# Kernel optimization log

Hardware: AMD Instinct MI355X
Metric: run time of the kernel (lower is better)

The kernel has to match this reference:

```python
import jax, jax.numpy as jnp
import numpy as np

N_NEWS, N_ENT, N_TOP = 100000, 50000, 2000
D = 128
N_EDGES = 1600000
HID, OUT = 512, 128


def setup_inputs() -> dict:
    key = jax.random.key(0)
    ks = jax.random.split(key, 12)
    return {
        "news_feats": jax.random.normal(ks[0], (N_NEWS, D), jnp.float32),
        "entity_feats": jax.random.normal(ks[1], (N_ENT, D), jnp.float32),
        "topic_feats": jax.random.normal(ks[2], (N_TOP, D), jnp.float32),
        "ent_row": jax.random.randint(ks[3], (N_EDGES,), 0, N_NEWS, jnp.int32),
        "ent_col": jax.random.randint(ks[4], (N_EDGES,), 0, N_ENT, jnp.int32),
        "top_row": jax.random.randint(ks[5], (N_EDGES,), 0, N_NEWS, jnp.int32),
        "top_col": jax.random.randint(ks[6], (N_EDGES,), 0, N_TOP, jnp.int32),
        "W1": jax.random.normal(ks[7], (3 * D, HID), jnp.float32) * 0.05,
        "b1": jnp.zeros((HID,), jnp.float32),
        "W2": jax.random.normal(ks[8], (HID, OUT), jnp.float32) * 0.05,
        "b2": jnp.zeros((OUT,), jnp.float32),
    }


def _agg(feats, row, col, num_news):
    # SpMM with binary adjacency: sum neighbor feats per news node
    gathered = feats[col]                                   # [E, D]
    summed = jax.ops.segment_sum(gathered, row, num_segments=num_news)
    deg = jax.ops.segment_sum(jnp.ones_like(row, dtype=feats.dtype), row,
                              num_segments=num_news)
    return summed / (deg[:, None] + 1e-8)


def reference(news_feats, entity_feats, topic_feats, ent_row, ent_col,
              top_row, top_col, W1, b1, W2, b2):
    n = news_feats.shape[0]
    ent_agg = _agg(entity_feats, ent_row, ent_col, n)
    top_agg = _agg(topic_feats, top_row, top_col, n)
    out = jnp.concatenate([news_feats, ent_agg, top_agg], axis=1)  # [N, 3D]
    h = jnp.tanh(out @ W1 + b1)
    return h @ W2 + b2
```

## Files before the change

kernel.cpp:

```cpp
#include <hip/hip_runtime.h>
#include <hip/hip_bf16.h>

#define NN 100000
#define NE 50000
#define NT 2000
#define DD 128
#define NEDGE 1600000
#define HID 512
#define OUTD 128
#define K1 (3*DD)
#define KX 256
#define NBKT 391

typedef __bf16 bf16x8 __attribute__((ext_vector_type(8)));
typedef __bf16 bf16x4 __attribute__((ext_vector_type(4)));
typedef float  f32x4  __attribute__((ext_vector_type(4)));

__device__ __forceinline__ __bf16 f2b(float f) {
    __hip_bfloat16 h = __float2bfloat16(f);
    union { __hip_bfloat16 h; __bf16 b; } u; u.h = h; return u.b;
}

__device__ __forceinline__ void gll16(const void* g, void* l) {
    __builtin_amdgcn_global_load_lds((const __attribute__((address_space(1))) void*)g,
                                     (__attribute__((address_space(3))) void*)l, 16, 0, 0);
}

__device__ __forceinline__ float ftanh(float x) {
    x = fminf(fmaxf(x, -15.f), 15.f);
    float t = __expf(2.f * x);
    return (t - 1.f) / (t + 1.f);
}

__global__ void conv_feats(const float* __restrict__ entf, const float* __restrict__ topf,
                           __bf16* __restrict__ entb, __bf16* __restrict__ topb) {
    long i = ((long)blockIdx.x * 256 + threadIdx.x) * 4;
    const long NEL = (long)NE * DD;
    if (i < NEL) {
        float4 v = *(const float4*)(entf + i);
        *(bf16x4*)(entb + i) = bf16x4{f2b(v.x), f2b(v.y), f2b(v.z), f2b(v.w)};
    } else {
        long j = i - NEL;
        float4 v = *(const float4*)(topf + j);
        *(bf16x4*)(topb + j) = bf16x4{f2b(v.x), f2b(v.y), f2b(v.z), f2b(v.w)};
    }
}

__global__ __launch_bounds__(256) void hist_buckets(const int* __restrict__ er,
                                                    const int* __restrict__ tr,
                                                    int* __restrict__ bc_e,
                                                    int* __restrict__ bc_t) {
    __shared__ int lhe[NBKT], lht[NBKT];
    const int tid = threadIdx.x;
    for (int i = tid; i < NBKT; i += 256) { lhe[i] = 0; lht[i] = 0; }
    __syncthreads();
    const int base = blockIdx.x * 8192;
    #pragma unroll 4
    for (int k = 0; k < 32; k++) {
        int e = base + k * 256 + tid;
        if (e < NEDGE) {
            atomicAdd(&lhe[er[e] >> 8], 1);
            atomicAdd(&lht[tr[e] >> 8], 1);
        }
    }
    __syncthreads();
    for (int i = tid; i < NBKT; i += 256) {
        if (lhe[i]) atomicAdd(&bc_e[i], lhe[i]);
        if (lht[i]) atomicAdd(&bc_t[i], lht[i]);
    }
}

__global__ void scan_buckets(int* __restrict__ bc_e, int* __restrict__ bc_t,
                             int* __restrict__ cur_e, int* __restrict__ cur_t,
                             int* __restrict__ offs_e, int* __restrict__ offs_t) {
    int* bc  = blockIdx.y ? bc_t : bc_e;
    int* cur = blockIdx.y ? cur_t : cur_e;
    int* offs = blockIdx.y ? offs_t : offs_e;
    __shared__ int s[512];
    int i = threadIdx.x;
    s[i] = (i < NBKT) ? bc[i] : 0;
    __syncthreads();
    #pragma unroll
    for (int off = 1; off < 512; off <<= 1) {
        int v = (i >= off) ? s[i - off] : 0;
        __syncthreads();
        s[i] += v;
        __syncthreads();
    }
    if (i < NBKT) {
        bc[i] = s[i];
        cur[i] = i ? s[i - 1] : 0;
    }
    if (i == 0) offs[0] = 0;
}

__global__ __launch_bounds__(256) void scatter_bucket(const int* __restrict__ er,
                                                      const int* __restrict__ ec,
                                                      const int* __restrict__ tr,
                                                      const int* __restrict__ tc,
                                                      int* __restrict__ cur_e,
                                                      int* __restrict__ cur_t,
                                                      int* __restrict__ be,
                                                      int* __restrict__ bt) {
    __shared__ int lhe[NBKT], lht[NBKT];
    __shared__ int lbe[NBKT], lbt[NBKT];
    const int tid = threadIdx.x;
    for (int i = tid; i < NBKT; i += 256) { lhe[i] = 0; lht[i] = 0; }
    __syncthreads();
    const int base = blockIdx.x * 4096;
    #pragma unroll 4
    for (int k = 0; k < 16; k++) {
        int e = base + k * 256 + tid;
        if (e < NEDGE) {
            atomicAdd(&lhe[er[e] >> 8], 1);
            atomicAdd(&lht[tr[e] >> 8], 1);
        }
    }
    __syncthreads();
    for (int i = tid; i < NBKT; i += 256) {
        int c = lhe[i];
        lbe[i] = c ? atomicAdd(&cur_e[i], c) : 0;
        lhe[i] = 0;
        c = lht[i];
        lbt[i] = c ? atomicAdd(&cur_t[i], c) : 0;
        lht[i] = 0;
    }
    __syncthreads();
    #pragma unroll 4
    for (int k = 0; k < 16; k++) {
        int e = base + k * 256 + tid;
        if (e < NEDGE) {
            int r = er[e];
            int b = r >> 8;
            int p = lbe[b] + atomicAdd(&lhe[b], 1);
            be[p] = ((r & 255) << 16) | ec[e];
            r = tr[e];
            b = r >> 8;
            p = lbt[b] + atomicAdd(&lht[b], 1);
            bt[p] = ((r & 255) << 16) | tc[e];
        }
    }
}

__global__ __launch_bounds__(256) void bucket_csr(const int* __restrict__ be,
                                                  const int* __restrict__ bt,
                                                  const int* __restrict__ bc_e,
                                                  const int* __restrict__ bc_t,
                                                  int* __restrict__ offs_e,
                                                  int* __restrict__ offs_t,
                                                  int* __restrict__ se,
                                                  int* __restrict__ st) {
    const int* buf = blockIdx.y ? bt : be;
    const int* bc  = blockIdx.y ? bc_t : bc_e;
    int* offs      = blockIdx.y ? offs_t : offs_e;
    int* sout      = blockIdx.y ? st : se;
    const int b = blockIdx.x;
    const int tid = threadIdx.x;
    const int start = b ? bc[b - 1] : 0;
    const int cnt = bc[b] - start;

    __shared__ int scn[256];
    __shared__ int lcur[256];
    scn[tid] = 0;
    __syncthreads();
    for (int i = tid; i < cnt; i += 256)
        atomicAdd(&scn[buf[start + i] >> 16], 1);
    __syncthreads();
    #pragma unroll
    for (int off = 1; off < 256; off <<= 1) {
        int v = (tid >= off) ? scn[tid - off] : 0;
        __syncthreads();
        scn[tid] += v;
        __syncthreads();
    }
    const int node = b * 256 + tid;
    if (node < NN) offs[node + 1] = start + scn[tid];
    lcur[tid] = start + (tid ? scn[tid - 1] : 0);
    __syncthreads();
    for (int i = tid; i < cnt; i += 256) {
        int v = buf[start + i];
        int p = atomicAdd(&lcur[v >> 16], 1);
        sout[p] = v & 0xFFFF;
    }
}

__global__ __launch_bounds__(256) void aggregate2(const __bf16* __restrict__ entb,
                                                  const __bf16* __restrict__ topb,
                                                  const int* __restrict__ offs_e,
                                                  const int* __restrict__ offs_t,
                                                  const int* __restrict__ se,
                                                  const int* __restrict__ st,
                                                  __bf16* __restrict__ X) {
    const int wave = threadIdx.x >> 6, lane = threadIdx.x & 63;
    const int node = blockIdx.x * 4 + wave;
    if (node >= NN) return;
    const int h = lane >> 4;
    const int d = (lane & 15) * 8;

    float ea[8] = {0,0,0,0,0,0,0,0};
    float pa[8] = {0,0,0,0,0,0,0,0};

    const int s0 = offs_e[node], s1 = offs_e[node + 1];
    int i = s0 + h;
    for (; i + 12 < s1; i += 16) {
        int c0 = se[i], c1 = se[i + 4], c2 = se[i + 8], c3 = se[i + 12];
        bf16x8 v0 = *(const bf16x8*)(entb + (long)c0 * DD + d);
        bf16x8 v1 = *(const bf16x8*)(entb + (long)c1 * DD + d);
        bf16x8 v2 = *(const bf16x8*)(entb + (long)c2 * DD + d);
        bf16x8 v3 = *(const bf16x8*)(entb + (long)c3 * DD + d);
        #pragma unroll
        for (int j = 0; j < 8; j++)
            ea[j] += ((float)v0[j] + (float)v1[j]) + ((float)v2[j] + (float)v3[j]);
    }
    for (; i < s1; i += 4) {
        bf16x8 v = *(const bf16x8*)(entb + (long)se[i] * DD + d);
        #pragma unroll
        for (int j = 0; j < 8; j++) ea[j] += (float)v[j];
    }

    const int t0 = offs_t[node], t1 = offs_t[node + 1];
    i = t0 + h;
    for (; i + 12 < t1; i += 16) {
        int c0 = st[i], c1 = st[i + 4], c2 = st[i + 8], c3 = st[i + 12];
        bf16x8 v0 = *(const bf16x8*)(topb + (long)c0 * DD + d);
        bf16x8 v1 = *(const bf16x8*)(topb + (long)c1 * DD + d);
        bf16x8 v2 = *(const bf16x8*)(topb + (long)c2 * DD + d);
        bf16x8 v3 = *(const bf16x8*)(topb + (long)c3 * DD + d);
        #pragma unroll
        for (int j = 0; j < 8; j++)
            pa[j] += ((float)v0[j] + (float)v1[j]) + ((float)v2[j] + (float)v3[j]);
    }
    for (; i < t1; i += 4) {
        bf16x8 v = *(const bf16x8*)(topb + (long)st[i] * DD + d);
        #pragma unroll
        for (int j = 0; j < 8; j++) pa[j] += (float)v[j];
    }

    #pragma unroll
    for (int j = 0; j < 8; j++) {
        ea[j] += __shfl_xor(ea[j], 16, 64);
        ea[j] += __shfl_xor(ea[j], 32, 64);
        pa[j] += __shfl_xor(pa[j], 16, 64);
        pa[j] += __shfl_xor(pa[j], 32, 64);
    }

    const float ie = 1.0f / ((float)(s1 - s0) + 1e-8f);
    const float it = 1.0f / ((float)(t1 - t0) + 1e-8f);
    __bf16* xr = X + (long)node * KX;
    if (h == 1) {
        *(bf16x8*)(xr + d) = bf16x8{f2b(ea[0]*ie), f2b(ea[1]*ie), f2b(ea[2]*ie), f2b(ea[3]*ie),
                                    f2b(ea[4]*ie), f2b(ea[5]*ie), f2b(ea[6]*ie), f2b(ea[7]*ie)};
    } else if (h == 2) {
        *(bf16x8*)(xr + DD + d) = bf16x8{f2b(pa[0]*it), f2b(pa[1]*it), f2b(pa[2]*it), f2b(pa[3]*it),
                                         f2b(pa[4]*it), f2b(pa[5]*it), f2b(pa[6]*it), f2b(pa[7]*it)};
    }
}

__global__ void conv_w(const float* __restrict__ W1, const float* __restrict__ W2,
                       __bf16* __restrict__ W1T, __bf16* __restrict__ W2T) {
    int i = blockIdx.x * 256 + threadIdx.x;
    if (i < K1 * HID) {
        int k = i / HID, n = i % HID;
        W1T[n * K1 + k] = f2b(W1[i]);
    } else {
        int j = i - K1 * HID;
        if (j < HID * OUTD) {
            int k = j / OUTD, n = j % OUTD;
            W2T[n * HID + k] = f2b(W2[j]);
        }
    }
}


__device__ __forceinline__ void stage_tile(const __bf16* __restrict__ src, int ldK,
                                           int k0, int row0, int rowmax,
                                           __bf16* lds, int w, int lane) {
    #pragma unroll
    for (int half = 0; half < 2; half++) {
        int ss = w * 64 + half * 256 + lane;
        int r = ss >> 2;
        int sw = (r & 3) ^ ((r >> 2) & 3);
        int c = (ss & 3) ^ sw;
        int gr = row0 + r; if (gr >= rowmax) gr = rowmax - 1;
        gll16(src + (long)gr * ldK + k0 + c * 8,
              lds + (w * 64 + half * 256) * 8);
    }
}

__device__ __forceinline__ void stage_tile_f32(const float* __restrict__ src, int ldK,
                                               int k0, int row0, int rowmax,
                                               __bf16* lds, int w, int lane) {
    #pragma unroll
    for (int half = 0; half < 2; half++) {
        int ss = w * 64 + half * 256 + lane;
        int r = ss >> 2;
        int sw = (r & 3) ^ ((r >> 2) & 3);
        int c = (ss & 3) ^ sw;
        int gr = row0 + r; if (gr >= rowmax) gr = rowmax - 1;
        const float* p = src + (long)gr * ldK + k0 + c * 8;
        float4 a = *(const float4*)p;
        float4 b = *(const float4*)(p + 4);
        *(bf16x8*)(lds + (long)ss * 8) = bf16x8{f2b(a.x), f2b(a.y), f2b(a.z), f2b(a.w),
                                                f2b(b.x), f2b(b.y), f2b(b.z), f2b(b.w)};
    }
}

__device__ __forceinline__ bf16x8 frag(const __bf16* lds, int r, int q) {
    int sw = (r & 3) ^ ((r >> 2) & 3);
    return *(const bf16x8*)(lds + (r * 4 + (q ^ sw)) * 8);
}

__device__ __forceinline__ void hs_write(__bf16* Hs, int r, int c, __bf16 v) {
    int ch = c >> 3;
    int pch = ((((ch >> 2) ^ ((r >> 2) & 3)) << 2) | ((ch & 3) ^ (r & 3)));
    Hs[(r * 16 + pch) * 8 + (c & 7)] = v;
}
__device__ __forceinline__ bf16x8 hs_frag(const __bf16* Hs, int r, int kk, int q) {
    int pch = (((kk ^ ((r >> 2) & 3)) << 2) | (q ^ (r & 3)));
    return *(const bf16x8*)(Hs + (r * 16 + pch) * 8);
}

__global__ __launch_bounds__(256, 2) void mlp_fused(const float* __restrict__ news,
                                                    const __bf16* __restrict__ X,
                                                    const __bf16* __restrict__ W1T,
                                                    const float* __restrict__ b1,
                                                    const __bf16* __restrict__ W2T,
                                                    const float* __restrict__ b2,
                                                    float* __restrict__ out) {
    __shared__ __bf16 Xs[128 * 32];
    __shared__ __bf16 Ws[128 * 32];
    __shared__ __bf16 Hs[128 * 128];
    const int bm = blockIdx.x * 128;
    const int t = threadIdx.x;
    const int lane = t & 63;
    const int w = t >> 6;
    const int quad = lane >> 4;
    const int l16 = lane & 15;
    const int wm = w >> 1, wn = w & 1;

    f32x4 oacc[4][4];
    #pragma unroll
    for (int i = 0; i < 4; i++)
        #pragma unroll
        for (int j = 0; j < 4; j++)
            #pragma unroll
            for (int r = 0; r < 4; r++) oacc[i][j][r] = 0.0f;

    for (int nc = 0; nc < 4; nc++) {
        f32x4 hacc[4][4];
        #pragma unroll
        for (int i = 0; i < 4; i++)
            #pragma unroll
            for (int j = 0; j < 4; j++)
                #pragma unroll
                for (int r = 0; r < 4; r++) hacc[i][j][r] = 0.0f;

        for (int kt = 0; kt < K1 / 32; kt++) {
            __syncthreads();
            if (kt < 4) stage_tile_f32(news, DD, kt * 32, bm, NN, Xs, w, lane);
            else        stage_tile(X, KX, (kt - 4) * 32, bm, NN, Xs, w, lane);
            stage_tile(W1T, K1, kt * 32, nc * 128, HID, Ws, w, lane);
            __syncthreads();
            bf16x8 af[4], bfr[4];
            #pragma unroll
            for (int i = 0; i < 4; i++) {
                af[i]  = frag(Xs, wm * 64 + i * 16 + l16, quad);
                bfr[i] = frag(Ws, wn * 64 + i * 16 + l16, quad);
            }
            #pragma unroll
            for (int i = 0; i < 4; i++)
                #pragma unroll
                for (int j = 0; j < 4; j++)
                    hacc[i][j] = __builtin_amdgcn_mfma_f32_16x16x32_bf16(af[i], bfr[j], hacc[i][j], 0, 0, 0);
        }

        #pragma unroll
        for (int j = 0; j < 4; j++) {
            const int col = wn * 64 + j * 16 + l16;
            const float bb = b1[nc * 128 + col];
            #pragma unroll
            for (int i = 0; i < 4; i++) {
                const int rbase = wm * 64 + i * 16 + quad * 4;
                #pragma unroll
                for (int r = 0; r < 4; r++)
                    hs_write(Hs, rbase + r, col, f2b(ftanh(hacc[i][j][r] + bb)));
            }
        }

        for (int kk = 0; kk < 4; kk++) {
            __syncthreads();
            stage_tile(W2T, HID, nc * 128 + kk * 32, 0, OUTD, Ws, w, lane);
            __syncthreads();
            bf16x8 af[4], bfr[4];
            #pragma unroll
            for (int i = 0; i < 4; i++) {
                af[i]  = hs_frag(Hs, wm * 64 + i * 16 + l16, kk, quad);
                bfr[i] = frag(Ws, wn * 64 + i * 16 + l16, quad);
            }
            #pragma unroll
            for (int i = 0; i < 4; i++)
                #pragma unroll
                for (int j = 0; j < 4; j++)
                    oacc[i][j] = __builtin_amdgcn_mfma_f32_16x16x32_bf16(af[i], bfr[j], oacc[i][j], 0, 0, 0);
        }
    }

    #pragma unroll
    for (int j = 0; j < 4; j++) {
        const int gc = wn * 64 + j * 16 + l16;
        const float bb = b2[gc];
        #pragma unroll
        for (int i = 0; i < 4; i++) {
            const int rbase = bm + wm * 64 + i * 16 + quad * 4;
            #pragma unroll
            for (int r = 0; r < 4; r++) {
                const int gr = rbase + r;
                if (gr < NN) out[(long)gr * OUTD + gc] = oacc[i][j][r] + bb;
            }
        }
    }
}

extern "C" void kernel_launch(void* const* d_in, const int* in_sizes, int n_in,
                              void* d_out, int out_size, void* d_ws, size_t ws_size,
                              hipStream_t stream) {
    const float* news  = (const float*)d_in[0];
    const float* ent_f = (const float*)d_in[1];
    const float* top_f = (const float*)d_in[2];
    const int* ent_row = (const int*)d_in[3];
    const int* ent_col = (const int*)d_in[4];
    const int* top_row = (const int*)d_in[5];
    const int* top_col = (const int*)d_in[6];
    const float* W1 = (const float*)d_in[7];
    const float* b1 = (const float*)d_in[8];
    const float* W2 = (const float*)d_in[9];
    const float* b2 = (const float*)d_in[10];

    char* ws = (char*)d_ws;
    int* offs_e = (int*)(ws + 0);
    int* offs_t = (int*)(ws + 400016);
    int* bc_e   = (int*)(ws + 800032);
    int* bc_t   = (int*)(ws + 801596);
    int* cur_e  = (int*)(ws + 803160);
    int* cur_t  = (int*)(ws + 804724);
    int* be     = (int*)(ws + 806320);
    int* bt     = (int*)(ws + 7206320);
    int* se     = (int*)(ws + 13606320);
    int* st     = (int*)(ws + 20006320);
    __bf16* entb = (__bf16*)(ws + 26406336);
    __bf16* topb = (__bf16*)(ws + 39206336);
    __bf16* X   = (__bf16*)(ws + 102400000);
    __bf16* W1T = (__bf16*)(ws + 179200000);
    __bf16* W2T = (__bf16*)(ws + 179593216);

    hipMemsetAsync(ws + 800032, 0, 6256, stream);
    conv_w<<<1024, 256, 0, stream>>>(W1, W2, W1T, W2T);
    conv_feats<<<6500, 256, 0, stream>>>(ent_f, top_f, entb, topb);
    hist_buckets<<<196, 256, 0, stream>>>(ent_row, top_row, bc_e, bc_t);
    scan_buckets<<<dim3(1, 2), 512, 0, stream>>>(bc_e, bc_t, cur_e, cur_t, offs_e, offs_t);
    scatter_bucket<<<392, 256, 0, stream>>>(ent_row, ent_col, top_row, top_col,
                                            cur_e, cur_t, be, bt);
    bucket_csr<<<dim3(NBKT, 2), 256, 0, stream>>>(be, bt, bc_e, bc_t,
                                                  offs_e, offs_t, se, st);
    aggregate2<<<NN / 4, 256, 0, stream>>>(entb, topb, offs_e, offs_t, se, st, X);
    mlp_fused<<<782, 256, 0, stream>>>(news, X, W1T, b1, W2T, b2, (float*)d_out);
}
```

Before: 561.0 us.

## Pre-convert news into X and double-buffer LDS staging in fused MLP

The news features are now converted to bf16 inside conv_feats and written into a widened X buffer (row stride 3*D). This lets the MLP kernel stage every K-tile through async global-to-LDS loads instead of doing fp32 loads and converting them on the fly. The fused MLP now double-buffers its X/W tiles in LDS and prefetches the next tile, including W2T and the next chunk's first W1 tile, while MFMAs run, with s_setprio raised around the MFMA blocks. The cost is a larger X buffer written and read (an extra 100000x128 bf16 round trip) and double the LDS for the staging tiles, which may reduce occupancy.

```diff
diff --git a/kernel.cpp b/kernel.cpp
--- a/kernel.cpp
+++ b/kernel.cpp
@@ -9,7 +9,6 @@
 #define HID 512
 #define OUTD 128
 #define K1 (3*DD)
-#define KX 256
 #define NBKT 391
 
 typedef __bf16 bf16x8 __attribute__((ext_vector_type(8)));
@@ -33,16 +32,24 @@
 }
 
 __global__ void conv_feats(const float* __restrict__ entf, const float* __restrict__ topf,
-                           __bf16* __restrict__ entb, __bf16* __restrict__ topb) {
+                           const float* __restrict__ news,
+                           __bf16* __restrict__ entb, __bf16* __restrict__ topb,
+                           __bf16* __restrict__ X) {
     long i = ((long)blockIdx.x * 256 + threadIdx.x) * 4;
     const long NEL = (long)NE * DD;
+    const long NTL = (long)NT * DD;
     if (i < NEL) {
         float4 v = *(const float4*)(entf + i);
         *(bf16x4*)(entb + i) = bf16x4{f2b(v.x), f2b(v.y), f2b(v.z), f2b(v.w)};
-    } else {
+    } else if (i < NEL + NTL) {
         long j = i - NEL;
         float4 v = *(const float4*)(topf + j);
         *(bf16x4*)(topb + j) = bf16x4{f2b(v.x), f2b(v.y), f2b(v.z), f2b(v.w)};
+    } else {
+        long j = i - NEL - NTL;
+        long row = j >> 7, col = j & 127;
+        float4 v = *(const float4*)(news + j);
+        *(bf16x4*)(X + row * K1 + col) = bf16x4{f2b(v.x), f2b(v.y), f2b(v.z), f2b(v.w)};
     }
 }
 
@@ -246,13 +253,13 @@
 
     const float ie = 1.0f / ((float)(s1 - s0) + 1e-8f);
     const float it = 1.0f / ((float)(t1 - t0) + 1e-8f);
-    __bf16* xr = X + (long)node * KX;
+    __bf16* xr = X + (long)node * K1;
     if (h == 1) {
-        *(bf16x8*)(xr + d) = bf16x8{f2b(ea[0]*ie), f2b(ea[1]*ie), f2b(ea[2]*ie), f2b(ea[3]*ie),
-                                    f2b(ea[4]*ie), f2b(ea[5]*ie), f2b(ea[6]*ie), f2b(ea[7]*ie)};
+        *(bf16x8*)(xr + DD + d) = bf16x8{f2b(ea[0]*ie), f2b(ea[1]*ie), f2b(ea[2]*ie), f2b(ea[3]*ie),
+                                         f2b(ea[4]*ie), f2b(ea[5]*ie), f2b(ea[6]*ie), f2b(ea[7]*ie)};
     } else if (h == 2) {
-        *(bf16x8*)(xr + DD + d) = bf16x8{f2b(pa[0]*it), f2b(pa[1]*it), f2b(pa[2]*it), f2b(pa[3]*it),
-                                         f2b(pa[4]*it), f2b(pa[5]*it), f2b(pa[6]*it), f2b(pa[7]*it)};
+        *(bf16x8*)(xr + 2*DD + d) = bf16x8{f2b(pa[0]*it), f2b(pa[1]*it), f2b(pa[2]*it), f2b(pa[3]*it),
+                                           f2b(pa[4]*it), f2b(pa[5]*it), f2b(pa[6]*it), f2b(pa[7]*it)};
     }
 }
 
@@ -287,24 +294,6 @@
     }
 }
 
-__device__ __forceinline__ void stage_tile_f32(const float* __restrict__ src, int ldK,
-                                               int k0, int row0, int rowmax,
-                                               __bf16* lds, int w, int lane) {
-    #pragma unroll
-    for (int half = 0; half < 2; half++) {
-        int ss = w * 64 + half * 256 + lane;
-        int r = ss >> 2;
-        int sw = (r & 3) ^ ((r >> 2) & 3);
-        int c = (ss & 3) ^ sw;
-        int gr = row0 + r; if (gr >= rowmax) gr = rowmax - 1;
-        const float* p = src + (long)gr * ldK + k0 + c * 8;
-        float4 a = *(const float4*)p;
-        float4 b = *(const float4*)(p + 4);
-        *(bf16x8*)(lds + (long)ss * 8) = bf16x8{f2b(a.x), f2b(a.y), f2b(a.z), f2b(a.w),
-                                                f2b(b.x), f2b(b.y), f2b(b.z), f2b(b.w)};
-    }
-}
-
 __device__ __forceinline__ bf16x8 frag(const __bf16* lds, int r, int q) {
     int sw = (r & 3) ^ ((r >> 2) & 3);
     return *(const bf16x8*)(lds + (r * 4 + (q ^ sw)) * 8);
@@ -320,15 +309,14 @@
     return *(const bf16x8*)(Hs + (r * 16 + pch) * 8);
 }
 
-__global__ __launch_bounds__(256, 2) void mlp_fused(const float* __restrict__ news,
-                                                    const __bf16* __restrict__ X,
+__global__ __launch_bounds__(256, 2) void mlp_fused(const __bf16* __restrict__ X,
                                                     const __bf16* __restrict__ W1T,
                                                     const float* __restrict__ b1,
                                                     const __bf16* __restrict__ W2T,
                                                     const float* __restrict__ b2,
                                                     float* __restrict__ out) {
-    __shared__ __bf16 Xs[128 * 32];
-    __shared__ __bf16 Ws[128 * 32];
+    __shared__ __bf16 Xs[2][128 * 32];
+    __shared__ __bf16 Ws[2][128 * 32];
     __shared__ __bf16 Hs[128 * 128];
     const int bm = blockIdx.x * 128;
     const int t = threadIdx.x;
@@ -346,6 +334,11 @@
             #pragma unroll
             for (int r = 0; r < 4; r++) oacc[i][j][r] = 0.0f;
 
+    stage_tile(X,   K1, 0, bm, NN,  Xs[0], w, lane);
+    stage_tile(W1T, K1, 0, 0,  HID, Ws[0], w, lane);
+    int cur = 0;
+    __syncthreads();
+
     for (int nc = 0; nc < 4; nc++) {
         f32x4 hacc[4][4];
         #pragma unroll
@@ -355,23 +348,29 @@
                 #pragma unroll
                 for (int r = 0; r < 4; r++) hacc[i][j][r] = 0.0f;
 
-        for (int kt = 0; kt < K1 / 32; kt++) {
-            __syncthreads();
-            if (kt < 4) stage_tile_f32(news, DD, kt * 32, bm, NN, Xs, w, lane);
-            else        stage_tile(X, KX, (kt - 4) * 32, bm, NN, Xs, w, lane);
-            stage_tile(W1T, K1, kt * 32, nc * 128, HID, Ws, w, lane);
-            __syncthreads();
+        for (int kt = 0; kt < 12; kt++) {
+            const int nb = cur ^ 1;
+            if (kt < 11) {
+                stage_tile(X,   K1, (kt + 1) * 32, bm,       NN,  Xs[nb], w, lane);
+                stage_tile(W1T, K1, (kt + 1) * 32, nc * 128, HID, Ws[nb], w, lane);
+            } else {
+                stage_tile(W2T, HID, nc * 128, 0, OUTD, Ws[nb], w, lane);
+            }
             bf16x8 af[4], bfr[4];
             #pragma unroll
             for (int i = 0; i < 4; i++) {
-                af[i]  = frag(Xs, wm * 64 + i * 16 + l16, quad);
-                bfr[i] = frag(Ws, wn * 64 + i * 16 + l16, quad);
-            }
+                af[i]  = frag(Xs[cur], wm * 64 + i * 16 + l16, quad);
+                bfr[i] = frag(Ws[cur], wn * 64 + i * 16 + l16, quad);
+            }
+            __builtin_amdgcn_s_setprio(1);
             #pragma unroll
             for (int i = 0; i < 4; i++)
                 #pragma unroll
                 for (int j = 0; j < 4; j++)
                     hacc[i][j] = __builtin_amdgcn_mfma_f32_16x16x32_bf16(af[i], bfr[j], hacc[i][j], 0, 0, 0);
+            __builtin_amdgcn_s_setprio(0);
+            __syncthreads();
+            cur = nb;
         }
 
         #pragma unroll
@@ -386,36 +385,47 @@
                     hs_write(Hs, rbase + r, col, f2b(ftanh(hacc[i][j][r] + bb)));
             }
         }
+        __syncthreads();
 
         for (int kk = 0; kk < 4; kk++) {
-            __syncthreads();
-            stage_tile(W2T, HID, nc * 128 + kk * 32, 0, OUTD, Ws, w, lane);
-            __syncthreads();
+            const int nb = cur ^ 1;
+            if (kk < 3) {
+                stage_tile(W2T, HID, nc * 128 + (kk + 1) * 32, 0, OUTD, Ws[nb], w, lane);
+            } else if (nc < 3) {
+                stage_tile(X,   K1, 0, bm,             NN,  Xs[nb], w, lane);
+                stage_tile(W1T, K1, 0, (nc + 1) * 128, HID, Ws[nb], w, lane);
+            }
             bf16x8 af[4], bfr[4];
             #pragma unroll
             for (int i = 0; i < 4; i++) {
                 af[i]  = hs_frag(Hs, wm * 64 + i * 16 + l16, kk, quad);
-                bfr[i] = frag(Ws, wn * 64 + i * 16 + l16, quad);
-            }
+                bfr[i] = frag(Ws[cur], wn * 64 + i * 16 + l16, quad);
+            }
+            __builtin_amdgcn_s_setprio(1);
             #pragma unroll
             for (int i = 0; i < 4; i++)
                 #pragma unroll
                 for (int j = 0; j < 4; j++)
                     oacc[i][j] = __builtin_amdgcn_mfma_f32_16x16x32_bf16(af[i], bfr[j], oacc[i][j], 0, 0, 0);
-        }
-    }
-
-    #pragma unroll
-    for (int j = 0; j < 4; j++) {
-        const int gc = wn * 64 + j * 16 + l16;
-        const float bb = b2[gc];
-        #pragma unroll
-        for (int i = 0; i < 4; i++) {
-            const int rbase = bm + wm * 64 + i * 16 + quad * 4;
-            #pragma unroll
-            for (int r = 0; r < 4; r++) {
-                const int gr = rbase + r;
-                if (gr < NN) out[(long)gr * OUTD + gc] = oacc[i][j][r] + bb;
+            __builtin_amdgcn_s_setprio(0);
+            __syncthreads();
+            cur = nb;
+        }
+    }
+
+    float bb[4];
+    #pragma unroll
+    for (int j = 0; j < 4; j++) bb[j] = b2[wn * 64 + j * 16 + l16];
+    #pragma unroll
+    for (int i = 0; i < 4; i++) {
+        #pragma unroll
+        for (int r = 0; r < 4; r++) {
+            const int gr = bm + wm * 64 + i * 16 + quad * 4 + r;
+            if (gr < NN) {
+                float* orow = out + (long)gr * OUTD + wn * 64 + l16;
+                #pragma unroll
+                for (int j = 0; j < 4; j++)
+                    orow[j * 16] = oacc[i][j][r] + bb[j];
             }
         }
     }
@@ -455,7 +465,7 @@
 
     hipMemsetAsync(ws + 800032, 0, 6256, stream);
     conv_w<<<1024, 256, 0, stream>>>(W1, W2, W1T, W2T);
-    conv_feats<<<6500, 256, 0, stream>>>(ent_f, top_f, entb, topb);
+    conv_feats<<<19000, 256, 0, stream>>>(ent_f, top_f, news, entb, topb, X);
     hist_buckets<<<196, 256, 0, stream>>>(ent_row, top_row, bc_e, bc_t);
     scan_buckets<<<dim3(1, 2), 512, 0, stream>>>(bc_e, bc_t, cur_e, cur_t, offs_e, offs_t);
     scatter_bucket<<<392, 256, 0, stream>>>(ent_row, ent_col, top_row, top_col,
@@ -463,5 +473,5 @@
     bucket_csr<<<dim3(NBKT, 2), 256, 0, stream>>>(be, bt, bc_e, bc_t,
                                                   offs_e, offs_t, se, st);
     aggregate2<<<NN / 4, 256, 0, stream>>>(entb, topb, offs_e, offs_t, se, st, X);
-    mlp_fused<<<782, 256, 0, stream>>>(news, X, W1T, b1, W2T, b2, (float*)d_out);
-}
+    mlp_fused<<<782, 256, 0, stream>>>(X, W1T, b1, W2T, b2, (float*)d_out);
+}
```

Result: faster. 540.4 us (-3.7%).
